# Optimization experiments

Hardware: AMD Instinct MI355X
Metric: run time of the kernel (lower is better)

Reference implementation:

```python
import jax, jax.numpy as jnp
import numpy as np

T, DIM, AH, HID, E = 2048, 1024, 2048, 1024, 8
N_HEADS, HEAD_DIM = 16, 128
N_GROUPS, TOPK_GROUPS, TOPK = 4, 2, 1
ROUTE_SCALE = 1.0


def rmsnorm(x, w, eps=1e-6):
    xf = x.astype(jnp.float32)
    var = jnp.mean(xf * xf, axis=-1, keepdims=True)
    return (xf * jax.lax.rsqrt(var + eps)).astype(x.dtype) * w


def setup_inputs() -> dict:
    key = jax.random.key(0)
    ks = jax.random.split(key, 12)

    def xavier(k, fan_in, fan_out, gain=1.0):
        lim = gain * np.sqrt(6.0 / (fan_in + fan_out))
        return jax.random.uniform(k, (fan_in, fan_out), minval=-lim, maxval=lim, dtype=jnp.float32)

    return {
        "x": jax.random.normal(ks[0], (T, DIM), dtype=jnp.float32),
        "x_projected": jax.random.normal(ks[1], (T, AH), dtype=jnp.float32),
        "attn_norm_w": jnp.ones((AH,), dtype=jnp.float32),
        # stored as [in, out] (transposed vs torch Linear)
        "wq": 0.02 * jax.random.normal(ks[2], (AH, N_HEADS * HEAD_DIM), dtype=jnp.float32),
        "bq": jnp.zeros((N_HEADS * HEAD_DIM,), dtype=jnp.float32),
        "wk": 0.02 * jax.random.normal(ks[3], (AH, N_HEADS * HEAD_DIM), dtype=jnp.float32),
        "bk": jnp.zeros((N_HEADS * HEAD_DIM,), dtype=jnp.float32),
        "q_norm_w": jnp.ones((HEAD_DIM,), dtype=jnp.float32),
        "k_norm_w": jnp.ones((HEAD_DIM,), dtype=jnp.float32),
        "w1": xavier(ks[4], DIM, HID),
        "b1": jnp.zeros((HID,), dtype=jnp.float32),
        "w2": xavier(ks[5], HID, HID),
        "b2": jnp.zeros((HID,), dtype=jnp.float32),
        "w3": xavier(ks[6], HID, E, gain=0.1),
        "b3": jnp.zeros((E,), dtype=jnp.float32),
    }


def reference(x, x_projected, attn_norm_w, wq, bq, wk, bk, q_norm_w, k_norm_w,
              w1, b1, w2, b2, w3, b3):
    t = x.shape[0]
    # ---- attention probe (torch.no_grad -> stop_gradient) ----
    xn = rmsnorm(x_projected, attn_norm_w)                      # [T, AH]
    q = (xn @ wq + bq).reshape(t, N_HEADS, HEAD_DIM)
    k = (xn @ wk + bk).reshape(t, N_HEADS, HEAD_DIM)
    q = rmsnorm(q, q_norm_w)
    k = rmsnorm(k, k_norm_w)
    scores = jnp.einsum('qhd,khd->hqk', q, k) / np.float32(np.sqrt(HEAD_DIM))
    probs = jax.nn.softmax(scores, axis=-1)                     # [H, T, T]
    # sum over query axis, mean over heads -> attention received per token
    importance = jax.lax.stop_gradient(probs.sum(axis=1).mean(axis=0))  # [T]

    # ---- router MLP (eval mode: dropout = identity) ----
    h = jax.nn.gelu(x @ w1 + b1, approximate=False)
    h = jax.nn.gelu(h @ w2 + b2, approximate=False)
    logits = h @ w3 + b3                                        # [T, E]
    r_scores = jax.nn.softmax(logits, axis=-1)

    # ---- grouped top-k (group-limited top-1 routing) ----
    sg = r_scores.reshape(t, N_GROUPS, E // N_GROUPS)
    group_scores = sg.max(axis=-1)                              # [T, G]
    _, gidx = jax.lax.top_k(group_scores, TOPK_GROUPS)          # [T, kg]
    mask = jnp.zeros((t, N_GROUPS), dtype=bool).at[jnp.arange(t)[:, None], gidx].set(True)
    masked = jnp.where(mask[:, :, None], sg, -jnp.inf).reshape(t, E)
    _, idx = jax.lax.top_k(masked, TOPK)                        # [T, 1]
    weights = jnp.take_along_axis(r_scores, idx, axis=1) * ROUTE_SCALE  # [T, 1]
    return weights, idx, importance
```

## Files before the change

kernel.cpp:

```cpp
#include <hip/hip_runtime.h>

#define T_TOK 2048
#define DIMX  1024
#define AHX   2048
#define HIDX  1024
#define NEXP  8
#define NHEAD 16
#define HD    128

typedef unsigned short us;
typedef short bf16x8 __attribute__((ext_vector_type(8)));
typedef float f32x4  __attribute__((ext_vector_type(4)));

__device__ __forceinline__ us f2bf(float f){
  unsigned int u = __builtin_bit_cast(unsigned int, f);
  u += 0x7FFFu + ((u >> 16) & 1u);
  return (us)(u >> 16);
}
__device__ __forceinline__ float bf2f(us h){
  unsigned int u = ((unsigned int)h) << 16;
  return __builtin_bit_cast(float, u);
}
__device__ __forceinline__ float gelu_exact(float x){
  return 0.5f * x * (1.0f + erff(x * 0.70710678118654752440f));
}
__device__ __forceinline__ void gload16(const us* g, us* l){
  __builtin_amdgcn_global_load_lds((const __attribute__((address_space(1))) unsigned int*)g,
                                   (__attribute__((address_space(3))) unsigned int*)l, 16, 0, 0);
}

__global__ __launch_bounds__(256) void k_pre(const float* __restrict__ x,
                                             us* __restrict__ xh, us* __restrict__ xl,
                                             const float* __restrict__ xproj,
                                             const float* __restrict__ anw,
                                             us* __restrict__ xn,
                                             const float* __restrict__ wq,
                                             const float* __restrict__ wk,
                                             us* __restrict__ wqkT,
                                             const float* __restrict__ w1,
                                             const float* __restrict__ w2,
                                             us* __restrict__ w1h, us* __restrict__ w1l,
                                             us* __restrict__ w2h, us* __restrict__ w2l){
  __shared__ float tile[32][33];
  __shared__ float ps[4];
  int bx = blockIdx.x, t = threadIdx.x;
  if (bx < 8192){
    int i = bx * 256 + t;
    float v = x[i];
    us h = f2bf(v);
    xh[i] = h;
    xl[i] = f2bf(v - bf2f(h));
    return;
  }
  if (bx < 10240){
    int row = bx - 8192;
    const float* p = xproj + (size_t)row * AHX;
    float v[8];
    *(float4*)&v[0] = *(const float4*)(p + t * 8);
    *(float4*)&v[4] = *(const float4*)(p + t * 8 + 4);
    float s = 0.f;
    #pragma unroll
    for (int i = 0; i < 8; i++) s += v[i] * v[i];
    #pragma unroll
    for (int m = 1; m < 64; m <<= 1) s += __shfl_xor(s, m);
    if ((t & 63) == 0) ps[t >> 6] = s;
    __syncthreads();
    float tot = ps[0] + ps[1] + ps[2] + ps[3];
    float rs = rsqrtf(tot * (1.0f / AHX) + 1e-6f);
    #pragma unroll
    for (int i = 0; i < 8; i++)
      xn[(size_t)row * AHX + t * 8 + i] = f2bf(v[i] * rs * anw[t * 8 + i]);
    return;
  }
  int tx = t & 31, ty = t >> 5;
  if (bx < 18432){
    int sub = bx - 10240;
    const float* in = (sub >> 12) ? wk : wq;
    us* o = wqkT + (size_t)(sub >> 12) * AHX * AHX;
    int rem = sub & 4095;
    int tbx = (rem & 63) * 32, tby = (rem >> 6) * 32;
    #pragma unroll
    for (int i = 0; i < 32; i += 8)
      tile[ty + i][tx] = in[(size_t)(tby + ty + i) * AHX + tbx + tx];
    __syncthreads();
    #pragma unroll
    for (int i = 0; i < 32; i += 8)
      o[(size_t)(tbx + ty + i) * AHX + tby + tx] = f2bf(tile[tx][ty + i]);
    return;
  }
  {
    int sub = bx - 18432;
    const float* in = (sub >> 10) ? w2 : w1;
    us* oh = (sub >> 10) ? w2h : w1h;
    us* ol = (sub >> 10) ? w2l : w1l;
    int rem = sub & 1023;
    int tbx = (rem & 31) * 32, tby = (rem >> 5) * 32;
    #pragma unroll
    for (int i = 0; i < 32; i += 8)
      tile[ty + i][tx] = in[(size_t)(tby + ty + i) * HIDX + tbx + tx];
    __syncthreads();
    #pragma unroll
    for (int i = 0; i < 32; i += 8){
      float v = tile[tx][ty + i];
      us h = f2bf(v);
      size_t o = (size_t)(tbx + ty + i) * DIMX + tby + tx;
      oh[o] = h;
      ol[o] = f2bf(v - bf2f(h));
    }
  }
}

__global__ __launch_bounds__(512) void k_gemm_qk(
    const us* __restrict__ A, const us* __restrict__ B,
    const float* __restrict__ bq, const float* __restrict__ bk,
    const float* __restrict__ qnw, const float* __restrict__ knw,
    us* __restrict__ Qnn, us* __restrict__ Knn, int K)
{
  __shared__ __align__(16) us sA[2][128 * 64];
  __shared__ __align__(16) us sB[2][128 * 64];
  __shared__ float sums[128][4];
  int tid = threadIdx.x;
  int bm = blockIdx.y * 128;
  int bnB = blockIdx.x * 128;
  int w = tid >> 6, l = tid & 63;
  int wm = (w >> 2) * 64, wn = (w & 3) * 32;
  int lhi = l >> 4, llo = l & 15;
  int srow = l >> 3;
  int scol = ((l & 7) ^ srow) * 8;
  int swz = llo & 7;

  const us* pA = &A[(size_t)(bm + w * 16 + srow) * K + scol];
  const us* pB = &B[(size_t)(bnB + w * 16 + srow) * K + scol];

  f32x4 acc[4][2] = {};

  #pragma unroll
  for (int i = 0; i < 2; i++){
    gload16(pA + (size_t)i * 8 * K, &sA[0][(w * 16 + i * 8) * 64]);
    gload16(pB + (size_t)i * 8 * K, &sB[0][(w * 16 + i * 8) * 64]);
  }
  __syncthreads();

  int cur = 0;
  for (int k0 = 0; k0 < K; k0 += 64){
    if (k0 + 64 < K){
      #pragma unroll
      for (int i = 0; i < 2; i++){
        gload16(pA + (size_t)i * 8 * K + k0 + 64, &sA[cur ^ 1][(w * 16 + i * 8) * 64]);
        gload16(pB + (size_t)i * 8 * K + k0 + 64, &sB[cur ^ 1][(w * 16 + i * 8) * 64]);
      }
    }
    bf16x8 af[2][4], bfr[2][2];
    #pragma unroll
    for (int kk = 0; kk < 2; kk++){
      int ca = ((kk * 4 + lhi) ^ swz) * 8;
      #pragma unroll
      for (int m = 0; m < 4; m++)
        af[kk][m] = *(const bf16x8*)&sA[cur][(wm + m * 16 + llo) * 64 + ca];
      #pragma unroll
      for (int n = 0; n < 2; n++)
        bfr[kk][n] = *(const bf16x8*)&sB[cur][(wn + n * 16 + llo) * 64 + ca];
    }
    #pragma unroll
    for (int kk = 0; kk < 2; kk++)
      #pragma unroll
      for (int m = 0; m < 4; m++)
        #pragma unroll
        for (int n = 0; n < 2; n++)
          acc[m][n] = __builtin_amdgcn_mfma_f32_16x16x32_bf16(af[kk][m], bfr[kk][n], acc[m][n], 0, 0, 0);
    __syncthreads();
    cur ^= 1;
  }

  bool isq = blockIdx.x < 16;
  const float* bias = isq ? bq : bk;
  const float* nw   = isq ? qnw : knw;
  us* outp = isq ? Qnn : Knn;
  int hcol0 = (blockIdx.x & 15) * 128;

  #pragma unroll
  for (int n = 0; n < 2; n++){
    float bv = bias[hcol0 + wn + n * 16 + llo];
    #pragma unroll
    for (int m = 0; m < 4; m++)
      #pragma unroll
      for (int j = 0; j < 4; j++) acc[m][n][j] += bv;
  }
  #pragma unroll
  for (int m = 0; m < 4; m++)
    #pragma unroll
    for (int j = 0; j < 4; j++){
      float p = 0.f;
      #pragma unroll
      for (int n = 0; n < 2; n++) p += acc[m][n][j] * acc[m][n][j];
      p += __shfl_xor(p, 1); p += __shfl_xor(p, 2);
      p += __shfl_xor(p, 4); p += __shfl_xor(p, 8);
      if (llo == 0) sums[wm + m * 16 + lhi * 4 + j][w & 3] = p;
    }
  __syncthreads();
  #pragma unroll
  for (int m = 0; m < 4; m++)
    #pragma unroll
    for (int j = 0; j < 4; j++){
      int row = wm + m * 16 + lhi * 4 + j;
      float rs = rsqrtf((sums[row][0] + sums[row][1] + sums[row][2] + sums[row][3]) * (1.0f / HD) + 1e-6f);
      #pragma unroll
      for (int n = 0; n < 2; n++){
        int col = wn + n * 16 + llo;
        outp[(size_t)(bm + row) * AHX + hcol0 + col] = f2bf(acc[m][n][j] * rs * nw[col]);
      }
    }
}

template<int EPI>
__global__ __launch_bounds__(256) void k_gemm_mlp(
    const us* __restrict__ Ah_, const us* __restrict__ Al_,
    const us* __restrict__ Bh_, const us* __restrict__ Bl_,
    const float* __restrict__ bias,
    float* __restrict__ Cf, us* __restrict__ Ch, us* __restrict__ Cl,
    int N, int K)
{
  __shared__ __align__(16) us sAh[2][64 * 64], sAl[2][64 * 64];
  __shared__ __align__(16) us sBh[2][64 * 64], sBl[2][64 * 64];
  int tid = threadIdx.x;
  int bm = blockIdx.y * 64, bn = blockIdx.x * 64;
  int w = tid >> 6, l = tid & 63;
  int wm = (w >> 1) * 32, wn = (w & 1) * 32;
  int lhi = l >> 4, llo = l & 15;
  int srow = l >> 3;
  int scol = ((l & 7) ^ srow) * 8;
  int swz = llo & 7;

  const us* pAh = &Ah_[(size_t)(bm + w * 8 + srow) * K + scol];
  const us* pAl = &Al_[(size_t)(bm + w * 8 + srow) * K + scol];
  const us* pBh = &Bh_[(size_t)(bn + w * 8 + srow) * K + scol];
  const us* pBl = &Bl_[(size_t)(bn + w * 8 + srow) * K + scol];

  f32x4 acc[2][2] = {};

  auto stage = [&](int buf, int k0){
    #pragma unroll
    for (int i = 0; i < 2; i++){
      int rb = (i * 32 + w * 8) * 64;
      gload16(pAh + (size_t)i * 32 * K + k0, &sAh[buf][rb]);
      gload16(pAl + (size_t)i * 32 * K + k0, &sAl[buf][rb]);
      gload16(pBh + (size_t)i * 32 * K + k0, &sBh[buf][rb]);
      gload16(pBl + (size_t)i * 32 * K + k0, &sBl[buf][rb]);
    }
  };

  stage(0, 0);
  __syncthreads();

  int cur = 0;
  for (int k0 = 0; k0 < K; k0 += 64){
    if (k0 + 64 < K) stage(cur ^ 1, k0 + 64);
    bf16x8 ah[2][2], al[2][2], bh[2][2], bl[2][2];
    #pragma unroll
    for (int kk = 0; kk < 2; kk++){
      int ca = ((kk * 4 + lhi) ^ swz) * 8;
      #pragma unroll
      for (int m = 0; m < 2; m++){
        ah[kk][m] = *(const bf16x8*)&sAh[cur][(wm + m * 16 + llo) * 64 + ca];
        al[kk][m] = *(const bf16x8*)&sAl[cur][(wm + m * 16 + llo) * 64 + ca];
        bh[kk][m] = *(const bf16x8*)&sBh[cur][(wn + m * 16 + llo) * 64 + ca];
        bl[kk][m] = *(const bf16x8*)&sBl[cur][(wn + m * 16 + llo) * 64 + ca];
      }
    }
    #pragma unroll
    for (int kk = 0; kk < 2; kk++)
      #pragma unroll
      for (int m = 0; m < 2; m++)
        #pragma unroll
        for (int n = 0; n < 2; n++){
          acc[m][n] = __builtin_amdgcn_mfma_f32_16x16x32_bf16(ah[kk][m], bh[kk][n], acc[m][n], 0, 0, 0);
          acc[m][n] = __builtin_amdgcn_mfma_f32_16x16x32_bf16(ah[kk][m], bl[kk][n], acc[m][n], 0, 0, 0);
          acc[m][n] = __builtin_amdgcn_mfma_f32_16x16x32_bf16(al[kk][m], bh[kk][n], acc[m][n], 0, 0, 0);
        }
    __syncthreads();
    cur ^= 1;
  }

  #pragma unroll
  for (int m = 0; m < 2; m++)
    #pragma unroll
    for (int n = 0; n < 2; n++){
      int col = bn + wn + n * 16 + llo;
      float bv = bias[col];
      #pragma unroll
      for (int j = 0; j < 4; j++){
        int row = bm + wm + m * 16 + lhi * 4 + j;
        float v = acc[m][n][j] + bv;
        size_t off = (size_t)row * N + col;
        if constexpr (EPI == 1){
          float g = gelu_exact(v);
          us hh = f2bf(g);
          Ch[off] = hh;
          Cl[off] = f2bf(g - bf2f(hh));
        } else {
          Cf[off] = gelu_exact(v);
        }
      }
    }
}

__global__ __launch_bounds__(512) void k_z(const us* __restrict__ Qn,
                                           const us* __restrict__ Kn,
                                           float* __restrict__ zpart){
  __shared__ __align__(16) us sK[2][128 * 128];
  int h = blockIdx.y;
  int qb = blockIdx.x * 128;
  int tid = threadIdx.x, w = tid >> 6, l = tid & 63;
  int lhi = l >> 4, llo = l & 15;
  int wq = qb + w * 16;
  const float scale = 0.08838834764831845f;

  auto stageK = [&](int buf, int kt){
    #pragma unroll
    for (int i = 0; i < 4; i++){
      int rb = w * 16 + i * 4;
      int r = rb + lhi;
      int c = ((llo ^ (r & 7))) * 8;
      gload16(&Kn[(size_t)(kt + r) * AHX + h * HD + c], &sK[buf][rb * 128]);
    }
  };

  bf16x8 qf[4];
  #pragma unroll
  for (int kk = 0; kk < 4; kk++)
    qf[kk] = *(const bf16x8*)&Qn[(size_t)(wq + llo) * AHX + h * HD + kk * 32 + lhi * 8];

  float rz[4] = {};
  int kt0 = blockIdx.z * 256;

  stageK(0, kt0);
  __syncthreads();

  #pragma unroll
  for (int t = 0; t < 2; t++){
    if (t == 0) stageK(1, kt0 + 128);
    f32x4 acc[8] = {};
    #pragma unroll
    for (int n = 0; n < 8; n++){
      int row = n * 16 + llo;
      #pragma unroll
      for (int kk = 0; kk < 4; kk++){
        bf16x8 kf = *(const bf16x8*)&sK[t][row * 128 + ((kk * 32 + lhi * 8) ^ ((llo & 7) << 3))];
        acc[n] = __builtin_amdgcn_mfma_f32_16x16x32_bf16(qf[kk], kf, acc[n], 0, 0, 0);
      }
    }
    #pragma unroll
    for (int j = 0; j < 4; j++){
      float s = 0.f;
      #pragma unroll
      for (int n = 0; n < 8; n++) s += __expf(acc[n][j] * scale);
      rz[j] += s;
    }
    if (t == 0) __syncthreads();
  }
  #pragma unroll
  for (int j = 0; j < 4; j++){
    float s = rz[j];
    s += __shfl_xor(s, 1); s += __shfl_xor(s, 2);
    s += __shfl_xor(s, 4); s += __shfl_xor(s, 8);
    if (llo == 0){
      int row = wq + lhi * 4 + j;
      zpart[(size_t)blockIdx.z * (NHEAD * T_TOK) + h * T_TOK + row] = s;
    }
  }
}

__global__ __launch_bounds__(512) void k_imp(const us* __restrict__ Qn,
                                             const us* __restrict__ Kn,
                                             const float* __restrict__ zpart,
                                             float* __restrict__ imp_part){
  __shared__ __align__(16) us sK[2][128 * 128];
  __shared__ float simp[8][128];
  int h = blockIdx.y;
  int qb = blockIdx.x * 128;
  int kt0 = blockIdx.z * 256;
  int tid = threadIdx.x, w = tid >> 6, l = tid & 63;
  int lhi = l >> 4, llo = l & 15;
  int wq = qb + w * 16;
  const float scale = 0.08838834764831845f;

  auto stageK = [&](int buf, int kt){
    #pragma unroll
    for (int i = 0; i < 4; i++){
      int rb = w * 16 + i * 4;
      int r = rb + lhi;
      int c = ((llo ^ (r & 7))) * 8;
      gload16(&Kn[(size_t)(kt + r) * AHX + h * HD + c], &sK[buf][rb * 128]);
    }
  };

  bf16x8 qf[4];
  float rcv[4];
  #pragma unroll
  for (int kk = 0; kk < 4; kk++)
    qf[kk] = *(const bf16x8*)&Qn[(size_t)(wq + llo) * AHX + h * HD + kk * 32 + lhi * 8];
  #pragma unroll
  for (int j = 0; j < 4; j++){
    int row = wq + lhi * 4 + j;
    float zs = 0.f;
    #pragma unroll
    for (int p = 0; p < 8; p++) zs += zpart[(size_t)p * (NHEAD * T_TOK) + h * T_TOK + row];
    rcv[j] = 1.0f / ((float)NHEAD * zs);
  }

  stageK(0, kt0);
  __syncthreads();

  #pragma unroll
  for (int t = 0; t < 2; t++){
    if (t == 0) stageK(1, kt0 + 128);
    f32x4 acc[8] = {};
    #pragma unroll
    for (int n = 0; n < 8; n++){
      int row = n * 16 + llo;
      #pragma unroll
      for (int kk = 0; kk < 4; kk++){
        bf16x8 kf = *(const bf16x8*)&sK[t][row * 128 + ((kk * 32 + lhi * 8) ^ ((llo & 7) << 3))];
        acc[n] = __builtin_amdgcn_mfma_f32_16x16x32_bf16(qf[kk], kf, acc[n], 0, 0, 0);
      }
    }
    #pragma unroll
    for (int n = 0; n < 8; n++){
      float s = 0.f;
      #pragma unroll
      for (int j = 0; j < 4; j++)
        s += __expf(acc[n][j] * scale) * rcv[j];
      s += __shfl_xor(s, 16);
      s += __shfl_xor(s, 32);
      if (l < 16) simp[w][n * 16 + l] = s;
    }
    __syncthreads();
    if (tid < 128){
      float tot = 0.f;
      #pragma unroll
      for (int ww = 0; ww < 8; ww++) tot += simp[ww][tid];
      imp_part[((size_t)blockIdx.x * NHEAD + h) * T_TOK + kt0 + t * 128 + tid] = tot;
    }
    __syncthreads();
  }
}

__global__ __launch_bounds__(256) void k_final(const float* __restrict__ imp_part,
                                               const float* __restrict__ h2,
                                               const float* __restrict__ w3,
                                               const float* __restrict__ b3,
                                               float* __restrict__ out){
  if (blockIdx.x < 8){
    int col = blockIdx.x * 256 + threadIdx.x;
    float s = 0.f;
    for (int r = 0; r < 256; r++) s += imp_part[(size_t)r * T_TOK + col];
    out[2 * T_TOK + col] = s;
    return;
  }
  int t = (blockIdx.x - 8) * 4 + (threadIdx.x >> 6);
  int l = threadIdx.x & 63;
  const float* hp = h2 + (size_t)t * HIDX;
  float acc[NEXP] = {};
  for (int i = l; i < HIDX; i += 64){
    float hv = hp[i];
    const float* wr = w3 + (size_t)i * NEXP;
    #pragma unroll
    for (int e = 0; e < NEXP; e++) acc[e] = fmaf(hv, wr[e], acc[e]);
  }
  #pragma unroll
  for (int mk = 1; mk < 64; mk <<= 1)
    #pragma unroll
    for (int e = 0; e < NEXP; e++) acc[e] += __shfl_xor(acc[e], mk);
  if (l == 0){
    float lg[NEXP], mx = -__builtin_inff();
    #pragma unroll
    for (int e = 0; e < NEXP; e++){ lg[e] = acc[e] + b3[e]; mx = fmaxf(mx, lg[e]); }
    float Z = 0.f, p[NEXP];
    #pragma unroll
    for (int e = 0; e < NEXP; e++){ p[e] = expf(lg[e] - mx); Z += p[e]; }
    float invZ = 1.0f / Z;
    #pragma unroll
    for (int e = 0; e < NEXP; e++) p[e] *= invZ;
    float gs[4];
    #pragma unroll
    for (int g = 0; g < 4; g++) gs[g] = fmaxf(p[2 * g], p[2 * g + 1]);
    int g1 = 0;
    #pragma unroll
    for (int g = 1; g < 4; g++) if (gs[g] > gs[g1]) g1 = g;
    int g2 = -1; float g2v = -__builtin_inff();
    #pragma unroll
    for (int g = 0; g < 4; g++) if (g != g1 && gs[g] > g2v){ g2v = gs[g]; g2 = g; }
    int best = 0; float bv = -__builtin_inff();
    #pragma unroll
    for (int e = 0; e < NEXP; e++){
      int g = e >> 1;
      if ((g == g1 || g == g2) && p[e] > bv){ bv = p[e]; best = e; }
    }
    out[t]         = bv;
    out[T_TOK + t] = (float)best;
  }
}

extern "C" void kernel_launch(void* const* d_in, const int* in_sizes, int n_in,
                              void* d_out, int out_size, void* d_ws, size_t ws_size,
                              hipStream_t stream){
  const float* x     = (const float*)d_in[0];
  const float* xproj = (const float*)d_in[1];
  const float* anw   = (const float*)d_in[2];
  const float* wq    = (const float*)d_in[3];
  const float* bq    = (const float*)d_in[4];
  const float* wk    = (const float*)d_in[5];
  const float* bk    = (const float*)d_in[6];
  const float* qnw   = (const float*)d_in[7];
  const float* knw   = (const float*)d_in[8];
  const float* w1    = (const float*)d_in[9];
  const float* b1    = (const float*)d_in[10];
  const float* w2    = (const float*)d_in[11];
  const float* b2    = (const float*)d_in[12];
  const float* w3    = (const float*)d_in[13];
  const float* b3    = (const float*)d_in[14];
  float* out = (float*)d_out;

  char* ws = (char*)d_ws;
  const size_t MB = 1024 * 1024;
  us* xn      = (us*)(ws);
  us* wqkT    = (us*)(ws + 8 * MB);
  us* Qnn     = (us*)(ws + 24 * MB);
  us* Knn     = (us*)(ws + 32 * MB);
  float* zpart    = (float*)(ws + 40 * MB);
  float* imp_part = (float*)(ws + 42 * MB);
  us* xh      = (us*)(ws + 44 * MB);
  us* xl      = (us*)(ws + 48 * MB);
  us* w1Th    = (us*)(ws + 52 * MB);
  us* w1Tl    = (us*)(ws + 54 * MB);
  us* w2Th    = (us*)(ws + 56 * MB);
  us* w2Tl    = (us*)(ws + 58 * MB);
  us* h1h     = (us*)(ws + 60 * MB);
  us* h1l     = (us*)(ws + 64 * MB);
  float* h2   = (float*)(ws + 68 * MB);

  k_pre<<<20480, 256, 0, stream>>>(x, xh, xl, xproj, anw, xn,
                                   wq, wk, wqkT, w1, w2, w1Th, w1Tl, w2Th, w2Tl);

  k_gemm_qk<<<dim3(32, 16), 512, 0, stream>>>(xn, wqkT, bq, bk, qnw, knw, Qnn, Knn, AHX);

  k_z<<<dim3(16, NHEAD, 8), 512, 0, stream>>>(Qnn, Knn, zpart);
  k_imp<<<dim3(16, NHEAD, 8), 512, 0, stream>>>(Qnn, Knn, zpart, imp_part);

  k_gemm_mlp<1><<<dim3(HIDX / 64, T_TOK / 64), 256, 0, stream>>>(
      xh, xl, w1Th, w1Tl, b1, nullptr, h1h, h1l, HIDX, DIMX);
  k_gemm_mlp<2><<<dim3(HIDX / 64, T_TOK / 64), 256, 0, stream>>>(
      h1h, h1l, w2Th, w2Tl, b2, h2, nullptr, nullptr, HIDX, HIDX);

  k_final<<<8 + T_TOK / 4, 256, 0, stream>>>(imp_part, h2, w3, b3, out);

  (void)in_sizes; (void)n_in; (void)out_size; (void)ws_size;
}
```

Measured before the change: 181.7 us.

## Fuse softmax-normaliser and importance passes into one kernel; drop LDS staging in MLP GEMM

The separate normaliser (k_z) and importance (k_imp) kernels become a single k_scores kernel. Each block now handles one query tile and head, and loops over all keys twice: the first pass builds the softmax row sums, the second accumulates the normalised column sums. This removes the zpart buffer round-trip and one launch. The cost is a much smaller grid (256 blocks instead of 2048) and a longer serial loop per block. Separately, the split-bf16 MLP GEMM now loads fragments straight from global memory into registers instead of double-buffering through shared memory, which gives up tile reuse in LDS and relies on L1/L2 caching.

Measured after the change: 272.9 us. 50.2% more time.

```diff
diff --git a/kernel.cpp b/kernel.cpp
--- a/kernel.cpp
+++ b/kernel.cpp
@@ -213,83 +213,59 @@
 }
 
 template<int EPI>
-__global__ __launch_bounds__(256) void k_gemm_mlp(
+__global__ __launch_bounds__(256) void k_mlp(
     const us* __restrict__ Ah_, const us* __restrict__ Al_,
     const us* __restrict__ Bh_, const us* __restrict__ Bl_,
     const float* __restrict__ bias,
     float* __restrict__ Cf, us* __restrict__ Ch, us* __restrict__ Cl,
     int N, int K)
 {
-  __shared__ __align__(16) us sAh[2][64 * 64], sAl[2][64 * 64];
-  __shared__ __align__(16) us sBh[2][64 * 64], sBl[2][64 * 64];
   int tid = threadIdx.x;
-  int bm = blockIdx.y * 64, bn = blockIdx.x * 64;
   int w = tid >> 6, l = tid & 63;
-  int wm = (w >> 1) * 32, wn = (w & 1) * 32;
   int lhi = l >> 4, llo = l & 15;
-  int srow = l >> 3;
-  int scol = ((l & 7) ^ srow) * 8;
-  int swz = llo & 7;
-
-  const us* pAh = &Ah_[(size_t)(bm + w * 8 + srow) * K + scol];
-  const us* pAl = &Al_[(size_t)(bm + w * 8 + srow) * K + scol];
-  const us* pBh = &Bh_[(size_t)(bn + w * 8 + srow) * K + scol];
-  const us* pBl = &Bl_[(size_t)(bn + w * 8 + srow) * K + scol];
+  int bm = blockIdx.y * 64 + (w >> 1) * 32;
+  int bn = blockIdx.x * 64 + (w & 1) * 32;
+
+  const us* pAh = Ah_ + (size_t)(bm + llo) * K + lhi * 8;
+  const us* pAl = Al_ + (size_t)(bm + llo) * K + lhi * 8;
+  const us* pBh = Bh_ + (size_t)(bn + llo) * K + lhi * 8;
+  const us* pBl = Bl_ + (size_t)(bn + llo) * K + lhi * 8;
 
   f32x4 acc[2][2] = {};
 
-  auto stage = [&](int buf, int k0){
-    #pragma unroll
-    for (int i = 0; i < 2; i++){
-      int rb = (i * 32 + w * 8) * 64;
-      gload16(pAh + (size_t)i * 32 * K + k0, &sAh[buf][rb]);
-      gload16(pAl + (size_t)i * 32 * K + k0, &sAl[buf][rb]);
-      gload16(pBh + (size_t)i * 32 * K + k0, &sBh[buf][rb]);
-      gload16(pBl + (size_t)i * 32 * K + k0, &sBl[buf][rb]);
-    }
-  };
-
-  stage(0, 0);
-  __syncthreads();
-
-  int cur = 0;
   for (int k0 = 0; k0 < K; k0 += 64){
-    if (k0 + 64 < K) stage(cur ^ 1, k0 + 64);
     bf16x8 ah[2][2], al[2][2], bh[2][2], bl[2][2];
     #pragma unroll
-    for (int kk = 0; kk < 2; kk++){
-      int ca = ((kk * 4 + lhi) ^ swz) * 8;
-      #pragma unroll
-      for (int m = 0; m < 2; m++){
-        ah[kk][m] = *(const bf16x8*)&sAh[cur][(wm + m * 16 + llo) * 64 + ca];
-        al[kk][m] = *(const bf16x8*)&sAl[cur][(wm + m * 16 + llo) * 64 + ca];
-        bh[kk][m] = *(const bf16x8*)&sBh[cur][(wn + m * 16 + llo) * 64 + ca];
-        bl[kk][m] = *(const bf16x8*)&sBl[cur][(wn + m * 16 + llo) * 64 + ca];
-      }
-    }
+    for (int m = 0; m < 2; m++)
+      #pragma unroll
+      for (int kk = 0; kk < 2; kk++){
+        size_t oa = (size_t)(m * 16) * K + k0 + kk * 32;
+        ah[m][kk] = *(const bf16x8*)(pAh + oa);
+        al[m][kk] = *(const bf16x8*)(pAl + oa);
+        bh[m][kk] = *(const bf16x8*)(pBh + oa);
+        bl[m][kk] = *(const bf16x8*)(pBl + oa);
+      }
     #pragma unroll
     for (int kk = 0; kk < 2; kk++)
       #pragma unroll
       for (int m = 0; m < 2; m++)
         #pragma unroll
         for (int n = 0; n < 2; n++){
-          acc[m][n] = __builtin_amdgcn_mfma_f32_16x16x32_bf16(ah[kk][m], bh[kk][n], acc[m][n], 0, 0, 0);
-          acc[m][n] = __builtin_amdgcn_mfma_f32_16x16x32_bf16(ah[kk][m], bl[kk][n], acc[m][n], 0, 0, 0);
-          acc[m][n] = __builtin_amdgcn_mfma_f32_16x16x32_bf16(al[kk][m], bh[kk][n], acc[m][n], 0, 0, 0);
+          acc[m][n] = __builtin_amdgcn_mfma_f32_16x16x32_bf16(ah[m][kk], bh[n][kk], acc[m][n], 0, 0, 0);
+          acc[m][n] = __builtin_amdgcn_mfma_f32_16x16x32_bf16(ah[m][kk], bl[n][kk], acc[m][n], 0, 0, 0);
+          acc[m][n] = __builtin_amdgcn_mfma_f32_16x16x32_bf16(al[m][kk], bh[n][kk], acc[m][n], 0, 0, 0);
         }
-    __syncthreads();
-    cur ^= 1;
   }
 
   #pragma unroll
   for (int m = 0; m < 2; m++)
     #pragma unroll
     for (int n = 0; n < 2; n++){
-      int col = bn + wn + n * 16 + llo;
+      int col = bn + n * 16 + llo;
       float bv = bias[col];
       #pragma unroll
       for (int j = 0; j < 4; j++){
-        int row = bm + wm + m * 16 + lhi * 4 + j;
+        int row = bm + m * 16 + lhi * 4 + j;
         float v = acc[m][n][j] + bv;
         size_t off = (size_t)row * N + col;
         if constexpr (EPI == 1){
@@ -304,10 +280,11 @@
     }
 }
 
-__global__ __launch_bounds__(512) void k_z(const us* __restrict__ Qn,
-                                           const us* __restrict__ Kn,
-                                           float* __restrict__ zpart){
+__global__ __launch_bounds__(512) void k_scores(const us* __restrict__ Qn,
+                                                const us* __restrict__ Kn,
+                                                float* __restrict__ imp_part){
   __shared__ __align__(16) us sK[2][128 * 128];
+  __shared__ float simp[8][128];
   int h = blockIdx.y;
   int qb = blockIdx.x * 128;
   int tid = threadIdx.x, w = tid >> 6, l = tid & 63;
@@ -320,7 +297,7 @@
     for (int i = 0; i < 4; i++){
       int rb = w * 16 + i * 4;
       int r = rb + lhi;
-      int c = ((llo ^ (r & 7))) * 8;
+      int c = (llo ^ (r & 7)) * 8;
       gload16(&Kn[(size_t)(kt + r) * AHX + h * HD + c], &sK[buf][rb * 128]);
     }
   };
@@ -331,117 +308,61 @@
     qf[kk] = *(const bf16x8*)&Qn[(size_t)(wq + llo) * AHX + h * HD + kk * 32 + lhi * 8];
 
   float rz[4] = {};
-  int kt0 = blockIdx.z * 256;
-
-  stageK(0, kt0);
+  float rcv[4] = {};
+
+  stageK(0, 0);
   __syncthreads();
 
-  #pragma unroll
-  for (int t = 0; t < 2; t++){
-    if (t == 0) stageK(1, kt0 + 128);
+  for (int t = 0; t < 32; t++){
+    int cur = t & 1;
+    if (t + 1 < 32) stageK(cur ^ 1, ((t + 1) & 15) * 128);
     f32x4 acc[8] = {};
     #pragma unroll
     for (int n = 0; n < 8; n++){
       int row = n * 16 + llo;
       #pragma unroll
       for (int kk = 0; kk < 4; kk++){
-        bf16x8 kf = *(const bf16x8*)&sK[t][row * 128 + ((kk * 32 + lhi * 8) ^ ((llo & 7) << 3))];
+        bf16x8 kf = *(const bf16x8*)&sK[cur][row * 128 + ((kk * 32 + lhi * 8) ^ ((llo & 7) << 3))];
         acc[n] = __builtin_amdgcn_mfma_f32_16x16x32_bf16(qf[kk], kf, acc[n], 0, 0, 0);
       }
     }
-    #pragma unroll
-    for (int j = 0; j < 4; j++){
-      float s = 0.f;
-      #pragma unroll
-      for (int n = 0; n < 8; n++) s += __expf(acc[n][j] * scale);
-      rz[j] += s;
-    }
-    if (t == 0) __syncthreads();
-  }
-  #pragma unroll
-  for (int j = 0; j < 4; j++){
-    float s = rz[j];
-    s += __shfl_xor(s, 1); s += __shfl_xor(s, 2);
-    s += __shfl_xor(s, 4); s += __shfl_xor(s, 8);
-    if (llo == 0){
-      int row = wq + lhi * 4 + j;
-      zpart[(size_t)blockIdx.z * (NHEAD * T_TOK) + h * T_TOK + row] = s;
-    }
-  }
-}
-
-__global__ __launch_bounds__(512) void k_imp(const us* __restrict__ Qn,
-                                             const us* __restrict__ Kn,
-                                             const float* __restrict__ zpart,
-                                             float* __restrict__ imp_part){
-  __shared__ __align__(16) us sK[2][128 * 128];
-  __shared__ float simp[8][128];
-  int h = blockIdx.y;
-  int qb = blockIdx.x * 128;
-  int kt0 = blockIdx.z * 256;
-  int tid = threadIdx.x, w = tid >> 6, l = tid & 63;
-  int lhi = l >> 4, llo = l & 15;
-  int wq = qb + w * 16;
-  const float scale = 0.08838834764831845f;
-
-  auto stageK = [&](int buf, int kt){
-    #pragma unroll
-    for (int i = 0; i < 4; i++){
-      int rb = w * 16 + i * 4;
-      int r = rb + lhi;
-      int c = ((llo ^ (r & 7))) * 8;
-      gload16(&Kn[(size_t)(kt + r) * AHX + h * HD + c], &sK[buf][rb * 128]);
-    }
-  };
-
-  bf16x8 qf[4];
-  float rcv[4];
-  #pragma unroll
-  for (int kk = 0; kk < 4; kk++)
-    qf[kk] = *(const bf16x8*)&Qn[(size_t)(wq + llo) * AHX + h * HD + kk * 32 + lhi * 8];
-  #pragma unroll
-  for (int j = 0; j < 4; j++){
-    int row = wq + lhi * 4 + j;
-    float zs = 0.f;
-    #pragma unroll
-    for (int p = 0; p < 8; p++) zs += zpart[(size_t)p * (NHEAD * T_TOK) + h * T_TOK + row];
-    rcv[j] = 1.0f / ((float)NHEAD * zs);
-  }
-
-  stageK(0, kt0);
-  __syncthreads();
-
-  #pragma unroll
-  for (int t = 0; t < 2; t++){
-    if (t == 0) stageK(1, kt0 + 128);
-    f32x4 acc[8] = {};
-    #pragma unroll
-    for (int n = 0; n < 8; n++){
-      int row = n * 16 + llo;
-      #pragma unroll
-      for (int kk = 0; kk < 4; kk++){
-        bf16x8 kf = *(const bf16x8*)&sK[t][row * 128 + ((kk * 32 + lhi * 8) ^ ((llo & 7) << 3))];
-        acc[n] = __builtin_amdgcn_mfma_f32_16x16x32_bf16(qf[kk], kf, acc[n], 0, 0, 0);
-      }
-    }
-    #pragma unroll
-    for (int n = 0; n < 8; n++){
-      float s = 0.f;
-      #pragma unroll
-      for (int j = 0; j < 4; j++)
-        s += __expf(acc[n][j] * scale) * rcv[j];
-      s += __shfl_xor(s, 16);
-      s += __shfl_xor(s, 32);
-      if (l < 16) simp[w][n * 16 + l] = s;
-    }
-    __syncthreads();
-    if (tid < 128){
-      float tot = 0.f;
-      #pragma unroll
-      for (int ww = 0; ww < 8; ww++) tot += simp[ww][tid];
-      imp_part[((size_t)blockIdx.x * NHEAD + h) * T_TOK + kt0 + t * 128 + tid] = tot;
-    }
-    __syncthreads();
+    if (t < 16){
+      #pragma unroll
+      for (int j = 0; j < 4; j++){
+        float s = 0.f;
+        #pragma unroll
+        for (int n = 0; n < 8; n++) s += __expf(acc[n][j] * scale);
+        rz[j] += s;
+      }
+      if (t == 15){
+        #pragma unroll
+        for (int j = 0; j < 4; j++){
+          float s = rz[j];
+          s += __shfl_xor(s, 1); s += __shfl_xor(s, 2);
+          s += __shfl_xor(s, 4); s += __shfl_xor(s, 8);
+          rcv[j] = 1.0f / ((float)NHEAD * s);
+        }
+      }
+      __syncthreads();
+    } else {
+      #pragma unroll
+      for (int n = 0; n < 8; n++){
+        float s = 0.f;
+        #pragma unroll
+        for (int j = 0; j < 4; j++) s += __expf(acc[n][j] * scale) * rcv[j];
+        s += __shfl_xor(s, 16);
+        s += __shfl_xor(s, 32);
+        if (l < 16) simp[w][n * 16 + l] = s;
+      }
+      __syncthreads();
+      if (tid < 128){
+        float tot = 0.f;
+        #pragma unroll
+        for (int ww = 0; ww < 8; ww++) tot += simp[ww][tid];
+        imp_part[((size_t)blockIdx.x * NHEAD + h) * T_TOK + (t - 16) * 128 + tid] = tot;
+      }
+      __syncthreads();
+    }
   }
 }
 
@@ -527,7 +448,6 @@
   us* wqkT    = (us*)(ws + 8 * MB);
   us* Qnn     = (us*)(ws + 24 * MB);
   us* Knn     = (us*)(ws + 32 * MB);
-  float* zpart    = (float*)(ws + 40 * MB);
   float* imp_part = (float*)(ws + 42 * MB);
   us* xh      = (us*)(ws + 44 * MB);
   us* xl      = (us*)(ws + 48 * MB);
@@ -544,12 +464,11 @@
 
   k_gemm_qk<<<dim3(32, 16), 512, 0, stream>>>(xn, wqkT, bq, bk, qnw, knw, Qnn, Knn, AHX);
 
-  k_z<<<dim3(16, NHEAD, 8), 512, 0, stream>>>(Qnn, Knn, zpart);
-  k_imp<<<dim3(16, NHEAD, 8), 512, 0, stream>>>(Qnn, Knn, zpart, imp_part);
-
-  k_gemm_mlp<1><<<dim3(HIDX / 64, T_TOK / 64), 256, 0, stream>>>(
+  k_scores<<<dim3(16, NHEAD), 512, 0, stream>>>(Qnn, Knn, imp_part);
+
+  k_mlp<1><<<dim3(HIDX / 64, T_TOK / 64), 256, 0, stream>>>(
       xh, xl, w1Th, w1Tl, b1, nullptr, h1h, h1l, HIDX, DIMX);
-  k_gemm_mlp<2><<<dim3(HIDX / 64, T_TOK / 64), 256, 0, stream>>>(
+  k_mlp<2><<<dim3(HIDX / 64, T_TOK / 64), 256, 0, stream>>>(
       h1h, h1l, w2Th, w2Tl, b2, h2, nullptr, nullptr, HIDX, HIDX);
 
   k_final<<<8 + T_TOK / 4, 256, 0, stream>>>(imp_part, h2, w3, b3, out);
```

## Enlarge attention-score tiles so each K tile feeds two query subtiles

Applied to the files above, without the earlier changes.

k_z and k_imp now give each block 256 queries and 512 keys instead of 128 and 256. Each wave holds two 16-row Q fragments, so every K fragment read from LDS feeds two MFMAs, and the K loop runs four double-buffered stages. The grid shrinks from 2048 to 512 blocks, and the zpart and imp_part reductions shrink to match. This cuts K reloads and LDS reads per MFMA, at the cost of more accumulator registers and fewer blocks to fill the 256 CUs.

Result: slower. 213.9 us (+17.7%).

```diff
diff --git a/kernel.cpp b/kernel.cpp
--- a/kernel.cpp
+++ b/kernel.cpp
@@ -309,10 +309,10 @@
                                            float* __restrict__ zpart){
   __shared__ __align__(16) us sK[2][128 * 128];
   int h = blockIdx.y;
-  int qb = blockIdx.x * 128;
+  int qb = blockIdx.x * 256;
   int tid = threadIdx.x, w = tid >> 6, l = tid & 63;
   int lhi = l >> 4, llo = l & 15;
-  int wq = qb + w * 16;
+  int wq = qb + w * 32;
   const float scale = 0.08838834764831845f;
 
   auto stageK = [&](int buf, int kt){
@@ -320,54 +320,62 @@
     for (int i = 0; i < 4; i++){
       int rb = w * 16 + i * 4;
       int r = rb + lhi;
-      int c = ((llo ^ (r & 7))) * 8;
+      int c = (llo ^ (r & 7)) * 8;
       gload16(&Kn[(size_t)(kt + r) * AHX + h * HD + c], &sK[buf][rb * 128]);
     }
   };
 
-  bf16x8 qf[4];
-  #pragma unroll
-  for (int kk = 0; kk < 4; kk++)
-    qf[kk] = *(const bf16x8*)&Qn[(size_t)(wq + llo) * AHX + h * HD + kk * 32 + lhi * 8];
-
-  float rz[4] = {};
-  int kt0 = blockIdx.z * 256;
+  bf16x8 qf[2][4];
+  #pragma unroll
+  for (int m = 0; m < 2; m++)
+    #pragma unroll
+    for (int kk = 0; kk < 4; kk++)
+      qf[m][kk] = *(const bf16x8*)&Qn[(size_t)(wq + m * 16 + llo) * AHX + h * HD + kk * 32 + lhi * 8];
+
+  float rz[2][4] = {};
+  int kt0 = blockIdx.z * 512;
 
   stageK(0, kt0);
   __syncthreads();
 
   #pragma unroll
-  for (int t = 0; t < 2; t++){
-    if (t == 0) stageK(1, kt0 + 128);
-    f32x4 acc[8] = {};
+  for (int t = 0; t < 4; t++){
+    int cur = t & 1;
+    if (t + 1 < 4) stageK(cur ^ 1, kt0 + (t + 1) * 128);
+    f32x4 acc[2][8] = {};
     #pragma unroll
     for (int n = 0; n < 8; n++){
       int row = n * 16 + llo;
       #pragma unroll
       for (int kk = 0; kk < 4; kk++){
-        bf16x8 kf = *(const bf16x8*)&sK[t][row * 128 + ((kk * 32 + lhi * 8) ^ ((llo & 7) << 3))];
-        acc[n] = __builtin_amdgcn_mfma_f32_16x16x32_bf16(qf[kk], kf, acc[n], 0, 0, 0);
-      }
-    }
+        bf16x8 kf = *(const bf16x8*)&sK[cur][row * 128 + ((kk * 32 + lhi * 8) ^ ((llo & 7) << 3))];
+        acc[0][n] = __builtin_amdgcn_mfma_f32_16x16x32_bf16(qf[0][kk], kf, acc[0][n], 0, 0, 0);
+        acc[1][n] = __builtin_amdgcn_mfma_f32_16x16x32_bf16(qf[1][kk], kf, acc[1][n], 0, 0, 0);
+      }
+    }
+    #pragma unroll
+    for (int m = 0; m < 2; m++)
+      #pragma unroll
+      for (int j = 0; j < 4; j++){
+        float s = 0.f;
+        #pragma unroll
+        for (int n = 0; n < 8; n++) s += __expf(acc[m][n][j] * scale);
+        rz[m][j] += s;
+      }
+    if (t + 1 < 4) __syncthreads();
+  }
+  #pragma unroll
+  for (int m = 0; m < 2; m++)
     #pragma unroll
     for (int j = 0; j < 4; j++){
-      float s = 0.f;
-      #pragma unroll
-      for (int n = 0; n < 8; n++) s += __expf(acc[n][j] * scale);
-      rz[j] += s;
-    }
-    if (t == 0) __syncthreads();
-  }
-  #pragma unroll
-  for (int j = 0; j < 4; j++){
-    float s = rz[j];
-    s += __shfl_xor(s, 1); s += __shfl_xor(s, 2);
-    s += __shfl_xor(s, 4); s += __shfl_xor(s, 8);
-    if (llo == 0){
-      int row = wq + lhi * 4 + j;
-      zpart[(size_t)blockIdx.z * (NHEAD * T_TOK) + h * T_TOK + row] = s;
-    }
-  }
+      float s = rz[m][j];
+      s += __shfl_xor(s, 1); s += __shfl_xor(s, 2);
+      s += __shfl_xor(s, 4); s += __shfl_xor(s, 8);
+      if (llo == 0){
+        int row = wq + m * 16 + lhi * 4 + j;
+        zpart[(size_t)blockIdx.z * (NHEAD * T_TOK) + h * T_TOK + row] = s;
+      }
+    }
 }
 
 __global__ __launch_bounds__(512) void k_imp(const us* __restrict__ Qn,
@@ -377,11 +385,11 @@
   __shared__ __align__(16) us sK[2][128 * 128];
   __shared__ float simp[8][128];
   int h = blockIdx.y;
-  int qb = blockIdx.x * 128;
-  int kt0 = blockIdx.z * 256;
+  int qb = blockIdx.x * 256;
+  int kt0 = blockIdx.z * 512;
   int tid = threadIdx.x, w = tid >> 6, l = tid & 63;
   int lhi = l >> 4, llo = l & 15;
-  int wq = qb + w * 16;
+  int wq = qb + w * 32;
   const float scale = 0.08838834764831845f;
 
   auto stageK = [&](int buf, int kt){
@@ -389,47 +397,55 @@
     for (int i = 0; i < 4; i++){
       int rb = w * 16 + i * 4;
       int r = rb + lhi;
-      int c = ((llo ^ (r & 7))) * 8;
+      int c = (llo ^ (r & 7)) * 8;
       gload16(&Kn[(size_t)(kt + r) * AHX + h * HD + c], &sK[buf][rb * 128]);
     }
   };
 
-  bf16x8 qf[4];
-  float rcv[4];
-  #pragma unroll
-  for (int kk = 0; kk < 4; kk++)
-    qf[kk] = *(const bf16x8*)&Qn[(size_t)(wq + llo) * AHX + h * HD + kk * 32 + lhi * 8];
-  #pragma unroll
-  for (int j = 0; j < 4; j++){
-    int row = wq + lhi * 4 + j;
-    float zs = 0.f;
-    #pragma unroll
-    for (int p = 0; p < 8; p++) zs += zpart[(size_t)p * (NHEAD * T_TOK) + h * T_TOK + row];
-    rcv[j] = 1.0f / ((float)NHEAD * zs);
-  }
+  bf16x8 qf[2][4];
+  float rcv[2][4];
+  #pragma unroll
+  for (int m = 0; m < 2; m++)
+    #pragma unroll
+    for (int kk = 0; kk < 4; kk++)
+      qf[m][kk] = *(const bf16x8*)&Qn[(size_t)(wq + m * 16 + llo) * AHX + h * HD + kk * 32 + lhi * 8];
+  #pragma unroll
+  for (int m = 0; m < 2; m++)
+    #pragma unroll
+    for (int j = 0; j < 4; j++){
+      int row = wq + m * 16 + lhi * 4 + j;
+      float zs = 0.f;
+      #pragma unroll
+      for (int p = 0; p < 4; p++) zs += zpart[(size_t)p * (NHEAD * T_TOK) + h * T_TOK + row];
+      rcv[m][j] = 1.0f / ((float)NHEAD * zs);
+    }
 
   stageK(0, kt0);
   __syncthreads();
 
   #pragma unroll
-  for (int t = 0; t < 2; t++){
-    if (t == 0) stageK(1, kt0 + 128);
-    f32x4 acc[8] = {};
+  for (int t = 0; t < 4; t++){
+    int cur = t & 1;
+    if (t + 1 < 4) stageK(cur ^ 1, kt0 + (t + 1) * 128);
+    f32x4 acc[2][8] = {};
     #pragma unroll
     for (int n = 0; n < 8; n++){
       int row = n * 16 + llo;
       #pragma unroll
       for (int kk = 0; kk < 4; kk++){
-        bf16x8 kf = *(const bf16x8*)&sK[t][row * 128 + ((kk * 32 + lhi * 8) ^ ((llo & 7) << 3))];
-        acc[n] = __builtin_amdgcn_mfma_f32_16x16x32_bf16(qf[kk], kf, acc[n], 0, 0, 0);
+        bf16x8 kf = *(const bf16x8*)&sK[cur][row * 128 + ((kk * 32 + lhi * 8) ^ ((llo & 7) << 3))];
+        acc[0][n] = __builtin_amdgcn_mfma_f32_16x16x32_bf16(qf[0][kk], kf, acc[0][n], 0, 0, 0);
+        acc[1][n] = __builtin_amdgcn_mfma_f32_16x16x32_bf16(qf[1][kk], kf, acc[1][n], 0, 0, 0);
       }
     }
     #pragma unroll
     for (int n = 0; n < 8; n++){
       float s = 0.f;
       #pragma unroll
-      for (int j = 0; j < 4; j++)
-        s += __expf(acc[n][j] * scale) * rcv[j];
+      for (int m = 0; m < 2; m++)
+        #pragma unroll
+        for (int j = 0; j < 4; j++)
+          s += __expf(acc[m][n][j] * scale) * rcv[m][j];
       s += __shfl_xor(s, 16);
       s += __shfl_xor(s, 32);
       if (l < 16) simp[w][n * 16 + l] = s;
@@ -453,7 +469,7 @@
   if (blockIdx.x < 8){
     int col = blockIdx.x * 256 + threadIdx.x;
     float s = 0.f;
-    for (int r = 0; r < 256; r++) s += imp_part[(size_t)r * T_TOK + col];
+    for (int r = 0; r < 128; r++) s += imp_part[(size_t)r * T_TOK + col];
     out[2 * T_TOK + col] = s;
     return;
   }
@@ -544,8 +560,8 @@
 
   k_gemm_qk<<<dim3(32, 16), 512, 0, stream>>>(xn, wqkT, bq, bk, qnw, knw, Qnn, Knn, AHX);
 
-  k_z<<<dim3(16, NHEAD, 8), 512, 0, stream>>>(Qnn, Knn, zpart);
-  k_imp<<<dim3(16, NHEAD, 8), 512, 0, stream>>>(Qnn, Knn, zpart, imp_part);
+  k_z<<<dim3(8, NHEAD, 4), 512, 0, stream>>>(Qnn, Knn, zpart);
+  k_imp<<<dim3(8, NHEAD, 4), 512, 0, stream>>>(Qnn, Knn, zpart, imp_part);
 
   k_gemm_mlp<1><<<dim3(HIDX / 64, T_TOK / 64), 256, 0, stream>>>(
       xh, xl, w1Th, w1Tl, b1, nullptr, h1h, h1l, HIDX, DIMX);
```
